# Performance work log

Hardware: AMD Instinct MI355X
Metric: run time of the kernel (lower is better)

## Reference

```python
import jax, jax.numpy as jnp
import numpy as np

MARGIN = 2.0


def setup_inputs() -> dict:
    key = jax.random.key(0)
    k1, k2 = jax.random.split(key)
    B, D, NUM_CLASSES = 8192, 128, 100
    features = jax.random.normal(k1, (B, D), dtype=jnp.float32)
    labels = jax.random.randint(k2, (B,), 0, NUM_CLASSES, dtype=jnp.int64)
    return {"features": features, "labels": labels}


def reference(features, labels):
    # Vectorized form of the O(B^2) nested-loop contrastive loss.
    B = features.shape[0]
    sq = jnp.sum(features * features, axis=-1)                      # [B]
    # squared pairwise L2 distances via the gram matrix
    d2 = sq[:, None] + sq[None, :] - 2.0 * (features @ features.T)  # [B, B]
    d2 = jnp.maximum(d2, 0.0)

    off_diag = ~jnp.eye(B, dtype=bool)
    same = labels[:, None] == labels[None, :]
    pos_mask = same & off_diag
    neg_mask = (~same) & off_diag

    # positive pairs contribute squared distance
    pos_loss = jnp.sum(jnp.where(pos_mask, d2, 0.0))

    # negative pairs contribute clamp(margin - dist, 0)^2; guard sqrt(0) grads
    d = jnp.sqrt(jnp.where(neg_mask, d2, 1.0))
    hinge = jnp.maximum(MARGIN - d, 0.0)
    neg_loss = jnp.sum(jnp.where(neg_mask, hinge * hinge, 0.0))

    pos_count = jnp.sum(pos_mask)
    total_pairs = jnp.asarray(B * (B - 1), dtype=d2.dtype)
    loss = pos_loss + neg_loss
    # original divides only when positive_pairs > 0
    return jnp.where(pos_count > 0, loss / total_pairs, loss)
```

## Files before the change

kernel.cpp:

```cpp
#include <hip/hip_runtime.h>
#include <hip/hip_bf16.h>


#define BN 8192
#define DD 128
#define NTILES 64
#define NBLOCKS (NTILES * (NTILES + 1) / 2)
#define SQ 26.0f
#define INV_S2 (1.0f / (26.0f * 26.0f))

typedef __attribute__((ext_vector_type(4))) int i32x4;

__global__ __launch_bounds__(256) void prep_kernel(const float* __restrict__ f,
        const int* __restrict__ labels, char* __restrict__ fbp,
        int2* __restrict__ meta) {
    const int tid = threadIdx.x;
    const int p = blockIdx.x;
    __shared__ __align__(16) char ls[16][144];

    const int r = tid >> 4;
    const int c = (tid & 15) * 8;
    const float* src = f + ((size_t)p * 16 + r) * DD + c;
    float4 a = *(const float4*)src;
    float4 b = *(const float4*)(src + 4);
    float rv[8] = {a.x, a.y, a.z, a.w, b.x, b.y, b.z, b.w};
    int s = 0;
#pragma unroll
    for (int j = 0; j < 8; j++) {
        int q = __float2int_rn(fminf(fmaxf(rv[j] * SQ, -127.f), 127.f));
        ls[r][c + j] = (char)q;
        s += q * q;
    }
#pragma unroll
    for (int off = 8; off > 0; off >>= 1) s += __shfl_down(s, off, 16);
    if ((tid & 15) == 0) meta[p * 16 + r] = make_int2(s, labels[p * 16 + r]);
    __syncthreads();

    if (tid < 128) {
        const int ks = tid >> 6, lane = tid & 63;
        const int l15 = lane & 15, quad = lane >> 4;
        i32x4 pack = *(const i32x4*)&ls[l15][ks * 64 + quad * 16];
        *(i32x4*)(fbp + ((size_t)(p * 2 + ks) * 64 + lane) * 16) = pack;
    }
}

__global__ __launch_bounds__(256) void pair_kernel(
        const char* __restrict__ fbp, const int2* __restrict__ meta,
        float2* __restrict__ partial) {
    const int t = blockIdx.x;
    int by = (int)((sqrtf(8.f * (float)t + 1.f) - 1.f) * 0.5f);
    while ((by + 1) * (by + 2) / 2 <= t) by++;
    while (by * (by + 1) / 2 > t) by--;
    const int bx = t - by * (by + 1) / 2;
    const bool diag = (bx == by);

    const int tid = threadIdx.x;
    const int wave = tid >> 6, lane = tid & 63;
    const int wx = wave & 1, wy = wave >> 1;
    const int i0 = bx * 128 + wy * 64;
    const int j0 = by * 128 + wx * 64;
    const int ip = i0 >> 4, jp = j0 >> 4;
    const int l15 = lane & 15, quad = lane >> 4;

    float pos = 0.f, neg = 0.f;

    if (!(diag && wx < wy)) {
        i32x4 acc4[4][4];
#pragma unroll
        for (int a = 0; a < 4; a++)
#pragma unroll
            for (int b = 0; b < 4; b++) acc4[a][b] = (i32x4){0, 0, 0, 0};

#pragma unroll
        for (int ks = 0; ks < 2; ks++) {
            i32x4 af[4], bg[4];
#pragma unroll
            for (int tt = 0; tt < 4; tt++)
                af[tt] = *(const i32x4*)(fbp +
                    ((size_t)((ip + tt) * 2 + ks) * 64 + lane) * 16);
#pragma unroll
            for (int tt = 0; tt < 4; tt++)
                bg[tt] = *(const i32x4*)(fbp +
                    ((size_t)((jp + tt) * 2 + ks) * 64 + lane) * 16);
#pragma unroll
            for (int m = 0; m < 4; m++)
#pragma unroll
                for (int n = 0; n < 4; n++)
                    acc4[m][n] = __builtin_amdgcn_mfma_i32_16x16x64_i8(
                        af[m], bg[n], acc4[m][n], 0, 0, 0);
        }

        int2 mj[4];
#pragma unroll
        for (int ni = 0; ni < 4; ni++) mj[ni] = meta[j0 + ni * 16 + l15];
        int2 mi[4][4];
#pragma unroll
        for (int m = 0; m < 4; m++)
#pragma unroll
            for (int r = 0; r < 4; r++) mi[m][r] = meta[i0 + m * 16 + quad * 4 + r];

        const bool strict = diag && (wx == wy);
#pragma unroll
        for (int m = 0; m < 4; m++)
#pragma unroll
            for (int n = 0; n < 4; n++)
#pragma unroll
                for (int r = 0; r < 4; r++) {
                    int il = m * 16 + quad * 4 + r;
                    int jl = n * 16 + l15;
                    bool valid = !strict || (il < jl);
                    int d2i = mi[m][r].x + mj[n].x - 2 * acc4[m][n][r];
                    float d2 = (float)d2i * INV_S2;
                    if (valid) {
                        if (mi[m][r].y == mj[n].y) pos += d2;
                        else if (d2 < 4.0f) {
                            float h = 2.0f - sqrtf(d2);
                            neg += h * h;
                        }
                    }
                }
    }

#pragma unroll
    for (int off = 32; off > 0; off >>= 1) {
        pos += __shfl_down(pos, off, 64);
        neg += __shfl_down(neg, off, 64);
    }
    __shared__ float red[2][4];
    if (lane == 0) { red[0][wave] = pos; red[1][wave] = neg; }
    __syncthreads();
    if (tid == 0)
        partial[t] = make_float2(red[0][0] + red[0][1] + red[0][2] + red[0][3],
                                 red[1][0] + red[1][1] + red[1][2] + red[1][3]);
}

__global__ __launch_bounds__(256) void reduce_kernel(
        const float2* __restrict__ partial, float* __restrict__ out) {
    const int tid = threadIdx.x;
    float p = 0.f, n = 0.f;
    for (int i = tid; i < NBLOCKS; i += 256) {
        float2 v = partial[i];
        p += v.x; n += v.y;
    }
#pragma unroll
    for (int off = 32; off > 0; off >>= 1) {
        p += __shfl_down(p, off, 64);
        n += __shfl_down(n, off, 64);
    }
    __shared__ float red[2][4];
    int lane = tid & 63, w = tid >> 6;
    if (lane == 0) { red[0][w] = p; red[1][w] = n; }
    __syncthreads();
    if (tid == 0) {
        float total = 2.0f * (red[0][0] + red[0][1] + red[0][2] + red[0][3] +
                              red[1][0] + red[1][1] + red[1][2] + red[1][3]);
        out[0] = total / 67100672.0f;
    }
}

extern "C" void kernel_launch(void* const* d_in, const int* in_sizes, int n_in,
                              void* d_out, int out_size, void* d_ws, size_t ws_size,
                              hipStream_t stream) {
    const float* f = (const float*)d_in[0];
    const int* labels = (const int*)d_in[1];
    float* out = (float*)d_out;

    char* fbp = (char*)d_ws;
    int2* meta = (int2*)((char*)d_ws + (size_t)BN * DD);
    float2* partial = (float2*)(meta + BN);

    prep_kernel<<<BN / 16, 256, 0, stream>>>(f, labels, fbp, meta);
    pair_kernel<<<NBLOCKS, 256, 0, stream>>>(fbp, meta, partial);
    reduce_kernel<<<1, 256, 0, stream>>>(partial, out);
}
```

Measured before the change: 85.31 us.

## Stage pair-kernel int8 tiles through LDS and accumulate positive loss in integers

The pair kernel now copies both 128-row int8 feature tiles into shared memory with direct global-to-LDS loads, then has each wave read its fragments from LDS instead of global memory. This cuts redundant global and L2 traffic, since waves that share a tile no longer fetch it separately, at the cost of 32KB of LDS per block and an extra barrier. The positive-pair sum is kept as an integer and scaled once at the end, and the hinge test compares the integer distance directly against a threshold. This saves a conversion and multiply per element, but relies on the integer sum not overflowing.

```diff
diff --git a/kernel.cpp b/kernel.cpp
--- a/kernel.cpp
+++ b/kernel.cpp
@@ -8,6 +8,7 @@
 #define NBLOCKS (NTILES * (NTILES + 1) / 2)
 #define SQ 26.0f
 #define INV_S2 (1.0f / (26.0f * 26.0f))
+#define D2I_HINGE 2704
 
 typedef __attribute__((ext_vector_type(4))) int i32x4;
 
@@ -59,8 +60,22 @@
     const int wx = wave & 1, wy = wave >> 1;
     const int i0 = bx * 128 + wy * 64;
     const int j0 = by * 128 + wx * 64;
-    const int ip = i0 >> 4, jp = j0 >> 4;
     const int l15 = lane & 15, quad = lane >> 4;
+
+    __shared__ __align__(16) char lds[32 * 1024];
+#pragma unroll
+    for (int q = 0; q < 8; q++) {
+        const int c = wave * 8 + q;
+        const int side = c >> 4;
+        const int cc = c & 15;
+        const char* g = fbp + ((size_t)((side ? by : bx) * 16 + cc)) * 1024
+                            + (size_t)lane * 16;
+        char* l = lds + (size_t)c * 1024;
+        __builtin_amdgcn_global_load_lds(
+            (const __attribute__((address_space(1))) void*)g,
+            (__attribute__((address_space(3))) void*)l, 16, 0, 0);
+    }
+    __syncthreads();
 
     float pos = 0.f, neg = 0.f;
 
@@ -71,17 +86,20 @@
 #pragma unroll
             for (int b = 0; b < 4; b++) acc4[a][b] = (i32x4){0, 0, 0, 0};
 
+        const char* la = lds;
+        const char* lb = lds + 16 * 1024;
+
 #pragma unroll
         for (int ks = 0; ks < 2; ks++) {
             i32x4 af[4], bg[4];
 #pragma unroll
             for (int tt = 0; tt < 4; tt++)
-                af[tt] = *(const i32x4*)(fbp +
-                    ((size_t)((ip + tt) * 2 + ks) * 64 + lane) * 16);
+                af[tt] = *(const i32x4*)(la +
+                    ((size_t)(((wy * 4 + tt) * 2 + ks) * 64 + lane)) * 16);
 #pragma unroll
             for (int tt = 0; tt < 4; tt++)
-                bg[tt] = *(const i32x4*)(fbp +
-                    ((size_t)((jp + tt) * 2 + ks) * 64 + lane) * 16);
+                bg[tt] = *(const i32x4*)(lb +
+                    ((size_t)(((wx * 4 + tt) * 2 + ks) * 64 + lane)) * 16);
 #pragma unroll
             for (int m = 0; m < 4; m++)
 #pragma unroll
@@ -90,16 +108,23 @@
                         af[m], bg[n], acc4[m][n], 0, 0, 0);
         }
 
-        int2 mj[4];
-#pragma unroll
-        for (int ni = 0; ni < 4; ni++) mj[ni] = meta[j0 + ni * 16 + l15];
-        int2 mi[4][4];
+        int w[4], lj[4];
+#pragma unroll
+        for (int n = 0; n < 4; n++) {
+            int2 m2 = meta[j0 + n * 16 + l15];
+            w[n] = m2.x; lj[n] = m2.y;
+        }
+        int u[4][4], li[4][4];
 #pragma unroll
         for (int m = 0; m < 4; m++)
 #pragma unroll
-            for (int r = 0; r < 4; r++) mi[m][r] = meta[i0 + m * 16 + quad * 4 + r];
+            for (int r = 0; r < 4; r++) {
+                int2 m2 = meta[i0 + m * 16 + quad * 4 + r];
+                u[m][r] = m2.x; li[m][r] = m2.y;
+            }
 
         const bool strict = diag && (wx == wy);
+        int posi = 0;
 #pragma unroll
         for (int m = 0; m < 4; m++)
 #pragma unroll
@@ -109,16 +134,16 @@
                     int il = m * 16 + quad * 4 + r;
                     int jl = n * 16 + l15;
                     bool valid = !strict || (il < jl);
-                    int d2i = mi[m][r].x + mj[n].x - 2 * acc4[m][n][r];
-                    float d2 = (float)d2i * INV_S2;
+                    int d2i = u[m][r] + w[n] - 2 * acc4[m][n][r];
                     if (valid) {
-                        if (mi[m][r].y == mj[n].y) pos += d2;
-                        else if (d2 < 4.0f) {
-                            float h = 2.0f - sqrtf(d2);
+                        if (li[m][r] == lj[n]) posi += d2i;
+                        else if (d2i < D2I_HINGE) {
+                            float h = 2.0f - sqrtf((float)d2i * INV_S2);
                             neg += h * h;
                         }
                     }
                 }
+        pos = (float)posi * INV_S2;
     }
 
 #pragma unroll
```

Measured after the change: 93.81 us. +10.0%, slower.

## Sort rows by label and skip hinge epilogue using a norm/dot lower bound

Applied to the files above, without the earlier changes.

A new single-block kernel counting-sorts rows by label, and the prep kernel reorders the quantized features and metadata to that order. Because the rows are sorted, most off-diagonal tiles have no same-label pairs, so those tiles skip the label comparisons. They also compute a conservative lower bound on the squared distance (min norms minus twice the max dot product) and skip the whole sqrt-based hinge epilogue when it cannot fall below the margin. This cuts the per-element epilogue arithmetic, which dominates the cheap int8 MFMA. The cost is an extra, mostly serial launch with shared-memory atomics, plus a gathered read in prep.

```diff
diff --git a/kernel.cpp b/kernel.cpp
--- a/kernel.cpp
+++ b/kernel.cpp
@@ -8,19 +8,40 @@
 #define NBLOCKS (NTILES * (NTILES + 1) / 2)
 #define SQ 26.0f
 #define INV_S2 (1.0f / (26.0f * 26.0f))
+#define D2I_HINGE 2704
 
 typedef __attribute__((ext_vector_type(4))) int i32x4;
 
+__global__ __launch_bounds__(256) void sort_kernel(
+        const int* __restrict__ labels, int* __restrict__ inv) {
+    __shared__ int hist[128];
+    const int tid = threadIdx.x;
+    if (tid < 128) hist[tid] = 0;
+    __syncthreads();
+    for (int i = tid; i < BN; i += 256) atomicAdd(&hist[labels[i]], 1);
+    __syncthreads();
+    if (tid == 0) {
+        int acc = 0;
+        for (int c = 0; c < 100; c++) { int h = hist[c]; hist[c] = acc; acc += h; }
+    }
+    __syncthreads();
+    for (int i = tid; i < BN; i += 256) {
+        int p = atomicAdd(&hist[labels[i]], 1);
+        inv[p] = i;
+    }
+}
+
 __global__ __launch_bounds__(256) void prep_kernel(const float* __restrict__ f,
-        const int* __restrict__ labels, char* __restrict__ fbp,
-        int2* __restrict__ meta) {
+        const int* __restrict__ labels, const int* __restrict__ inv,
+        char* __restrict__ fbp, int2* __restrict__ meta) {
     const int tid = threadIdx.x;
     const int p = blockIdx.x;
     __shared__ __align__(16) char ls[16][144];
 
     const int r = tid >> 4;
     const int c = (tid & 15) * 8;
-    const float* src = f + ((size_t)p * 16 + r) * DD + c;
+    const int oldr = inv[p * 16 + r];
+    const float* src = f + (size_t)oldr * DD + c;
     float4 a = *(const float4*)src;
     float4 b = *(const float4*)(src + 4);
     float rv[8] = {a.x, a.y, a.z, a.w, b.x, b.y, b.z, b.w};
@@ -33,7 +54,7 @@
     }
 #pragma unroll
     for (int off = 8; off > 0; off >>= 1) s += __shfl_down(s, off, 16);
-    if ((tid & 15) == 0) meta[p * 16 + r] = make_int2(s, labels[p * 16 + r]);
+    if ((tid & 15) == 0) meta[p * 16 + r] = make_int2(s, labels[oldr]);
     __syncthreads();
 
     if (tid < 128) {
@@ -90,35 +111,81 @@
                         af[m], bg[n], acc4[m][n], 0, 0, 0);
         }
 
-        int2 mj[4];
-#pragma unroll
-        for (int ni = 0; ni < 4; ni++) mj[ni] = meta[j0 + ni * 16 + l15];
-        int2 mi[4][4];
-#pragma unroll
-        for (int m = 0; m < 4; m++)
-#pragma unroll
-            for (int r = 0; r < 4; r++) mi[m][r] = meta[i0 + m * 16 + quad * 4 + r];
-
-        const bool strict = diag && (wx == wy);
-#pragma unroll
-        for (int m = 0; m < 4; m++)
-#pragma unroll
-            for (int n = 0; n < 4; n++)
-#pragma unroll
-                for (int r = 0; r < 4; r++) {
-                    int il = m * 16 + quad * 4 + r;
-                    int jl = n * 16 + l15;
-                    bool valid = !strict || (il < jl);
-                    int d2i = mi[m][r].x + mj[n].x - 2 * acc4[m][n][r];
-                    float d2 = (float)d2i * INV_S2;
-                    if (valid) {
-                        if (mi[m][r].y == mj[n].y) pos += d2;
-                        else if (d2 < 4.0f) {
-                            float h = 2.0f - sqrtf(d2);
-                            neg += h * h;
+        const int* lab32 = (const int*)meta;
+        const bool posable = diag ||
+            (lab32[2 * (bx * 128 + 127) + 1] == lab32[2 * (by * 128) + 1]);
+
+        if (posable) {
+            int2 mj[4];
+#pragma unroll
+            for (int ni = 0; ni < 4; ni++) mj[ni] = meta[j0 + ni * 16 + l15];
+            int2 mi[4][4];
+#pragma unroll
+            for (int m = 0; m < 4; m++)
+#pragma unroll
+                for (int r = 0; r < 4; r++)
+                    mi[m][r] = meta[i0 + m * 16 + quad * 4 + r];
+
+            const bool strict = diag && (wx == wy);
+#pragma unroll
+            for (int m = 0; m < 4; m++)
+#pragma unroll
+                for (int n = 0; n < 4; n++)
+#pragma unroll
+                    for (int r = 0; r < 4; r++) {
+                        int il = m * 16 + quad * 4 + r;
+                        int jl = n * 16 + l15;
+                        bool valid = !strict || (il < jl);
+                        int d2i = mi[m][r].x + mj[n].x - 2 * acc4[m][n][r];
+                        float d2 = (float)d2i * INV_S2;
+                        if (valid) {
+                            if (mi[m][r].y == mj[n].y) pos += d2;
+                            else if (d2 < 4.0f) {
+                                float h = 2.0f - sqrtf(d2);
+                                neg += h * h;
+                            }
                         }
                     }
-                }
+        } else {
+            int wn[4];
+#pragma unroll
+            for (int n = 0; n < 4; n++) wn[n] = lab32[2 * (j0 + n * 16 + l15)];
+            int un[4][4];
+#pragma unroll
+            for (int m = 0; m < 4; m++)
+#pragma unroll
+                for (int r = 0; r < 4; r++)
+                    un[m][r] = lab32[2 * (i0 + m * 16 + quad * 4 + r)];
+
+            int minu = 0x7fffffff, minw = 0x7fffffff, mx = (int)0x80000000;
+#pragma unroll
+            for (int m = 0; m < 4; m++)
+#pragma unroll
+                for (int r = 0; r < 4; r++) minu = min(minu, un[m][r]);
+#pragma unroll
+            for (int n = 0; n < 4; n++) minw = min(minw, wn[n]);
+#pragma unroll
+            for (int m = 0; m < 4; m++)
+#pragma unroll
+                for (int n = 0; n < 4; n++)
+#pragma unroll
+                    for (int r = 0; r < 4; r++) mx = max(mx, acc4[m][n][r]);
+
+            if (minu + minw - 2 * mx < D2I_HINGE) {
+#pragma unroll
+                for (int m = 0; m < 4; m++)
+#pragma unroll
+                    for (int n = 0; n < 4; n++)
+#pragma unroll
+                        for (int r = 0; r < 4; r++) {
+                            int d2i = un[m][r] + wn[n] - 2 * acc4[m][n][r];
+                            if (d2i < D2I_HINGE) {
+                                float h = 2.0f - sqrtf((float)d2i * INV_S2);
+                                neg += h * h;
+                            }
+                        }
+            }
+        }
     }
 
 #pragma unroll
@@ -168,8 +235,10 @@
     char* fbp = (char*)d_ws;
     int2* meta = (int2*)((char*)d_ws + (size_t)BN * DD);
     float2* partial = (float2*)(meta + BN);
-
-    prep_kernel<<<BN / 16, 256, 0, stream>>>(f, labels, fbp, meta);
+    int* inv = (int*)(partial + NBLOCKS);
+
+    sort_kernel<<<1, 256, 0, stream>>>(labels, inv);
+    prep_kernel<<<BN / 16, 256, 0, stream>>>(f, labels, inv, fbp, meta);
     pair_kernel<<<NBLOCKS, 256, 0, stream>>>(fbp, meta, partial);
     reduce_kernel<<<1, 256, 0, stream>>>(partial, out);
 }
```

Result: slower. 97.40 us (+14.2%).
